# Kernel tuning notes

Hardware: AMD Instinct MI355X
Metric: run time of the kernel (lower is better)

## Reference

```python
import jax, jax.numpy as jnp
import numpy as np

N_NODES = 50000
N_EDGES = 800000
NODE_DIM = 128
EDGE_DIM = 128
HIDDEN = 128
GATE_DIM = 2


def _mlp(x, w1, b1, w2, b2):
    # Linear -> ReLU -> Linear (assumed 2-layer MLP(in, out, hidden))
    return jax.nn.relu(x @ w1.T + b1) @ w2.T + b2


def _init_linear(key, out_d, in_d, scale=0.02):
    return (jax.random.normal(key, (out_d, in_d), dtype=jnp.float32) * scale)


def setup_inputs() -> dict:
    key = jax.random.key(0)
    ks = jax.random.split(key, 32)
    inp = {}
    inp["h_node"] = jax.random.normal(ks[0], (N_NODES, NODE_DIM), dtype=jnp.float32)
    inp["h_edge"] = jax.random.normal(ks[1], (N_EDGES, EDGE_DIM), dtype=jnp.float32)
    inp["edge_index"] = jax.random.randint(ks[2], (2, N_EDGES), 0, N_NODES, dtype=jnp.int64)
    inp["relative_vec"] = jax.random.normal(ks[3], (N_EDGES, 3), dtype=jnp.float32)
    inp["distance"] = jax.random.uniform(ks[4], (N_EDGES,), dtype=jnp.float32)
    inp["node_extra"] = jax.random.normal(ks[5], (N_NODES, GATE_DIM), dtype=jnp.float32)
    # left_lin_edge: MLP(node_dim, node_dim, hidden)
    inp["left_w1"] = _init_linear(ks[6], HIDDEN, NODE_DIM)
    inp["left_b1"] = jnp.zeros((HIDDEN,), jnp.float32)
    inp["left_w2"] = _init_linear(ks[7], NODE_DIM, HIDDEN)
    inp["left_b2"] = jnp.zeros((NODE_DIM,), jnp.float32)
    # right_lin_edge: MLP(node_dim, node_dim, hidden)
    inp["right_w1"] = _init_linear(ks[8], HIDDEN, NODE_DIM)
    inp["right_b1"] = jnp.zeros((HIDDEN,), jnp.float32)
    inp["right_w2"] = _init_linear(ks[9], NODE_DIM, HIDDEN)
    inp["right_b2"] = jnp.zeros((NODE_DIM,), jnp.float32)
    # BondFFN(edge_dim, node_dim*2, inter_dim=node_dim, gate_dim, out_dim=1)
    inp["bond_lin_w"] = _init_linear(ks[10], NODE_DIM, EDGE_DIM)           # bond_linear (no bias)
    inp["nodeb_lin_w"] = _init_linear(ks[11], NODE_DIM, 2 * NODE_DIM)      # node_linear (no bias)
    inp["inter_w1"] = _init_linear(ks[12], NODE_DIM, NODE_DIM)             # inter MLP(node_dim,1,node_dim)
    inp["inter_b1"] = jnp.zeros((NODE_DIM,), jnp.float32)
    inp["inter_w2"] = _init_linear(ks[13], 1, NODE_DIM)
    inp["inter_b2"] = jnp.zeros((1,), jnp.float32)
    gate_in = EDGE_DIM + 2 * NODE_DIM + GATE_DIM                            # 386
    inp["gate_w1"] = _init_linear(ks[14], 32, gate_in)                     # gate MLP(gate_in,1,32)
    inp["gate_b1"] = jnp.zeros((32,), jnp.float32)
    inp["gate_w2"] = _init_linear(ks[15], 1, 32)
    inp["gate_b2"] = jnp.zeros((1,), jnp.float32)
    # pos_scale_net: MLP(node_dim+1+2, 1, hidden) -> sigmoid
    inp["scale_w1"] = _init_linear(ks[16], HIDDEN, NODE_DIM + 1 + GATE_DIM)
    inp["scale_b1"] = jnp.zeros((HIDDEN,), jnp.float32)
    inp["scale_w2"] = _init_linear(ks[17], 1, HIDDEN)
    inp["scale_b2"] = jnp.zeros((1,), jnp.float32)
    return inp


def reference(h_node, h_edge, edge_index, relative_vec, distance, node_extra,
              left_w1, left_b1, left_w2, left_b2,
              right_w1, right_b1, right_w2, right_b2,
              bond_lin_w, nodeb_lin_w,
              inter_w1, inter_b1, inter_w2, inter_b2,
              gate_w1, gate_b1, gate_w2, gate_b2,
              scale_w1, scale_b1, scale_w2, scale_b2):
    el, er = edge_index[0], edge_index[1]
    # gather + per-edge node MLPs
    left_feat = _mlp(h_node[el], left_w1, left_b1, left_w2, left_b2)    # [E, node_dim]
    right_feat = _mlp(h_node[er], right_w1, right_b1, right_w2, right_b2)
    both_extra = node_extra[el]                                         # [E, gate_dim]
    node_cat = jnp.concatenate([left_feat, right_feat], axis=-1)        # [E, 2*node_dim]
    # BondFFN
    inter_feat = h_edge @ bond_lin_w.T + node_cat @ nodeb_lin_w.T       # [E, node_dim]
    inter_feat = _mlp(inter_feat, inter_w1, inter_b1, inter_w2, inter_b2)  # [E, 1]
    gate = _mlp(jnp.concatenate([h_edge, node_cat, both_extra], axis=-1),
                gate_w1, gate_b1, gate_w2, gate_b2)                     # [E, 1]
    weight_edge = inter_feat * jax.nn.sigmoid(gate)                     # [E, 1]
    d = distance[:, None]
    force_edge = weight_edge * relative_vec / (d + 1e-6) / (d + 5.0) * 5  # [E, 3]
    # scatter_sum over left node index
    delta_pos = jax.ops.segment_sum(force_edge, el, num_segments=h_node.shape[0])  # [N, 3]
    nrm = jnp.linalg.norm(delta_pos, axis=-1, keepdims=True)
    scale = jax.nn.sigmoid(_mlp(jnp.concatenate([h_node, node_extra, nrm], axis=-1),
                                scale_w1, scale_b1, scale_w2, scale_b2))  # [N, 1]
    return delta_pos * scale
```

## Files before the change

### kernel.cpp

```cpp
#include <hip/hip_runtime.h>
#include <math.h>

#define N_NODES 50000
#define N_EDGES 800000

using bf16x8 = __attribute__((ext_vector_type(8))) short;
using f32x4  = __attribute__((ext_vector_type(4))) float;
typedef unsigned short u16;
typedef unsigned int   u32;

__device__ __forceinline__ u16 f2bf(float f) {
    union { float f; u32 u; } v; v.f = f;
    u32 u = v.u + 0x7fffu + ((v.u >> 16) & 1u);
    return (u16)(u >> 16);
}
__device__ __forceinline__ float bf2f(u32 h) {
    union { u32 u; float f; } v; v.u = h << 16;
    return v.f;
}

#define SA_LD 136
#define SW_LD 40

template<bool RELU>
__global__ __launch_bounds__(256, 4)
void mfma_gemm(const u16* __restrict__ A, int lda,
               const u16* __restrict__ W, int ldw,
               const float* __restrict__ bias,
               u16* __restrict__ C, int ldc,
               int M, int N, int K)
{
    __shared__ u16 sA[64 * SW_LD];
    __shared__ u16 sW[64 * SW_LD];
    const int tid = threadIdx.x;
    const int w = tid >> 6, lane = tid & 63, lx = lane & 15, quad = lane >> 4;
    const int m0 = blockIdx.x * 64, n0 = blockIdx.y * 64;

    f32x4 acc[4];
#pragma unroll
    for (int nt = 0; nt < 4; ++nt) {
        float b = bias ? bias[n0 + nt * 16 + lx] : 0.f;
        f32x4 t; t[0] = b; t[1] = b; t[2] = b; t[3] = b; acc[nt] = t;
    }

    const int sr = tid >> 2;
    const int sseg = (tid & 3) * 8;
    const int ksteps = K >> 5;
    for (int ks = 0; ks < ksteps; ++ks) {
        const int k0 = ks * 32;
        __syncthreads();
        int am = m0 + sr; if (am >= M) am = M - 1;
        uint4 va = *(const uint4*)&A[(size_t)am * lda + k0 + sseg];
        *(uint4*)&sA[sr * SW_LD + sseg] = va;
        uint4 vw = *(const uint4*)&W[(size_t)(n0 + sr) * ldw + k0 + sseg];
        *(uint4*)&sW[sr * SW_LD + sseg] = vw;
        __syncthreads();
        bf16x8 af = *(const bf16x8*)&sA[(w * 16 + lx) * SW_LD + quad * 8];
#pragma unroll
        for (int nt = 0; nt < 4; ++nt) {
            bf16x8 bf = *(const bf16x8*)&sW[(nt * 16 + lx) * SW_LD + quad * 8];
            acc[nt] = __builtin_amdgcn_mfma_f32_16x16x32_bf16(af, bf, acc[nt], 0, 0, 0);
        }
    }
#pragma unroll
    for (int r = 0; r < 4; ++r) {
        int m = m0 + w * 16 + quad * 4 + r;
        if (m >= M) continue;
#pragma unroll
        for (int nt = 0; nt < 4; ++nt) {
            float v = acc[nt][r];
            if (RELU) v = fmaxf(v, 0.f);
            C[(size_t)m * ldc + n0 + nt * 16 + lx] = f2bf(v);
        }
    }
}

__global__ void conv_hnode(const float* __restrict__ src, u16* __restrict__ dst)
{
    int idx = blockIdx.x * 256 + threadIdx.x;
    if (idx >= N_NODES * 32) return;
    float4 v = ((const float4*)src)[idx];
    uint2 o;
    o.x = (u32)f2bf(v.x) | ((u32)f2bf(v.y) << 16);
    o.y = (u32)f2bf(v.z) | ((u32)f2bf(v.w) << 16);
    *(uint2*)&dst[(size_t)idx * 4] = o;
}

__global__ void prep_small(const float* lw1, const float* rw1,
                           const float* lb1, const float* rb1,
                           const float* bond_w, const float* iw1, const float* gw1,
                           const float* sw1,
                           u16* W1cat, float* b1cat, u16* bond_bf, u16* iw1_bf,
                           u16* gate_bf, u16* sw1c)
{
    int idx = blockIdx.x * 256 + threadIdx.x;
    if (idx < 32768) {
        int i = idx >> 7, k = idx & 127;
        float v = (i < 128) ? lw1[i * 128 + k] : rw1[(i - 128) * 128 + k];
        W1cat[idx] = f2bf(v);
    } else if (idx < 33024) {
        int i = idx - 32768;
        b1cat[i] = (i < 128) ? lb1[i] : rb1[i - 128];
    } else if (idx < 49408) {
        int t = idx - 33024;
        int e = t & 7, lx = (t >> 3) & 15, quad = (t >> 7) & 3;
        int ks = (t >> 9) & 3, g = t >> 11;
        int n = g * 16 + lx, k = ks * 32 + quad * 8 + e;
        bond_bf[t] = f2bf(bond_w[n * 128 + k]);
    } else if (idx < 65792) {
        int t = idx - 49408;
        int e = t & 7, lx = (t >> 3) & 15, quad = (t >> 7) & 3;
        int ks = (t >> 9) & 3, g = t >> 11;
        int n = g * 16 + lx, k = ks * 32 + quad * 8 + e;
        iw1_bf[t] = f2bf(iw1[n * 128 + k]);
    } else if (idx < 69888) {
        int t = idx - 65792;
        int e = t & 7, lx = (t >> 3) & 15, quad = (t >> 7) & 3;
        int ks = (t >> 9) & 3, g = t >> 11;
        int n = g * 16 + lx, k = ks * 32 + quad * 8 + e;
        gate_bf[t] = f2bf(gw1[(size_t)n * 386 + k]);
    } else if (idx < 90368) {
        int t = idx - 69888;
        int o = t / 160, k = t % 160;
        sw1c[t] = (k < 131) ? f2bf(sw1[(size_t)o * 131 + k]) : (u16)0;
    }
}

__global__ void compose_wp(const float* __restrict__ nodeb_w, const float* __restrict__ gw1,
                           const float* __restrict__ lw2, const float* __restrict__ rw2,
                           const float* __restrict__ lb2, const float* __restrict__ rb2,
                           const float* __restrict__ gb1,
                           u16* __restrict__ WP, float* __restrict__ bP)
{
    int idx = blockIdx.x * 256 + threadIdx.x;
    if (idx >= 320 * 256) return;
    int i = idx >> 8;
    int j = idx & 255;
    bool leftRow = (i < 160);
    bool leftK = (j < 128);
    if (leftRow != leftK) { WP[idx] = 0; return; }

    const float* src;
    const float* w2 = leftRow ? lw2 : rw2;
    const float* b2 = leftRow ? lb2 : rb2;
    float biasExtra = 0.f;
    if (i < 128) {
        int c = ((i & 7) << 4) + (i >> 3);
        src = nodeb_w + (size_t)c * 256;
    } else if (i < 160) {
        int r = i - 128, g = ((r & 1) << 4) + (r >> 1);
        src = gw1 + (size_t)g * 386 + 128;
        biasExtra = gb1[g];
    } else if (i < 288) {
        int r = i - 160, c = ((r & 7) << 4) + (r >> 3);
        src = nodeb_w + (size_t)c * 256 + 128;
    } else {
        int r = i - 288, g = ((r & 1) << 4) + (r >> 1);
        src = gw1 + (size_t)g * 386 + 256;
    }
    int jj = j & 127;
    float s = 0.f;
#pragma unroll 4
    for (int k = 0; k < 128; ++k)
        s += src[k] * w2[(size_t)k * 128 + jj];
    WP[idx] = f2bf(s);
    if (jj == 0) {
        float b = biasExtra;
        for (int k = 0; k < 128; ++k) b += src[k] * b2[k];
        bP[i] = b;
    }
}

__global__ void fix_glx(u16* __restrict__ P, const float* __restrict__ ne,
                        const float* __restrict__ gw1)
{
    int idx = blockIdx.x * 256 + threadIdx.x;
    if (idx >= N_NODES * 32) return;
    int n = idx >> 5, g = idx & 31;
    int pos = ((g & 15) << 1) + (g >> 4);
    u16* p = &P[(size_t)n * 320 + 128 + pos];
    float v = bf2f(*p) + ne[n * 2] * gw1[(size_t)g * 386 + 384]
                       + ne[n * 2 + 1] * gw1[(size_t)g * 386 + 385];
    *p = f2bf(v);
}

__global__ __launch_bounds__(512, 4)
void edge_kernel(const float* __restrict__ he,
                 const int*   __restrict__ eidx,
                 const float* __restrict__ rel_vec,
                 const float* __restrict__ dist,
                 const u16*   __restrict__ P,
                 const u16*   __restrict__ bondw,
                 const u16*   __restrict__ iw1w,
                 const u16*   __restrict__ gatew,
                 const float* __restrict__ ib1,
                 const float* __restrict__ iw2,
                 const float* __restrict__ ib2,
                 const float* __restrict__ gw2,
                 const float* __restrict__ gb2,
                 float* __restrict__ dp)
{
    __shared__ u16 sA[128 * SA_LD];
    __shared__ u16 sW[16384 + 4096];
    __shared__ int sEL[128], sER[128];
    __shared__ float sG[128], sIS[128];

    const int tid = threadIdx.x;
    const int w = tid >> 6, lane = tid & 63, lx = lane & 15, quad = lane >> 4;
    const int eb = blockIdx.x * 128;

    if (tid < 128) { sEL[tid] = eidx[eb + tid]; sER[tid] = eidx[N_EDGES + eb + tid]; }

#pragma unroll
    for (int j = 0; j < 4; ++j) {
        int t = j * 512 + tid;
        *(uint4*)&sW[t * 8] = *(const uint4*)&bondw[t * 8];
    }
    *(uint4*)&sW[16384 + tid * 8] = *(const uint4*)&gatew[tid * 8];

#pragma unroll
    for (int j = 0; j < 8; ++j) {
        int fid = j * 512 + tid;
        int e = fid >> 5, kq = (fid & 31) << 2;
        float4 v = *(const float4*)&he[(size_t)(eb + e) * 128 + kq];
        uint2 o;
        o.x = (u32)f2bf(v.x) | ((u32)f2bf(v.y) << 16);
        o.y = (u32)f2bf(v.z) | ((u32)f2bf(v.w) << 16);
        *(uint2*)&sA[e * SA_LD + kq] = o;
    }
    __syncthreads();

    uint4 lv[4], rv[4]; u32 gl[4], gr[4];
#pragma unroll
    for (int r = 0; r < 4; ++r) {
        int erow = w * 16 + quad * 4 + r;
        size_t lbase = (size_t)sEL[erow] * 320;
        size_t rbase = (size_t)sER[erow] * 320 + 160;
        lv[r] = *(const uint4*)&P[lbase + lx * 8];
        rv[r] = *(const uint4*)&P[rbase + lx * 8];
        gl[r] = *(const u32*)&P[lbase + 128 + lx * 2];
        gr[r] = *(const u32*)&P[rbase + 128 + lx * 2];
    }

    f32x4 acc[8], accg[2];
#pragma unroll
    for (int i = 0; i < 8; ++i) { f32x4 z; z[0]=0;z[1]=0;z[2]=0;z[3]=0; acc[i] = z; }
    { f32x4 z; z[0]=0;z[1]=0;z[2]=0;z[3]=0; accg[0] = z; accg[1] = z; }

#pragma unroll
    for (int ks = 0; ks < 4; ++ks) {
        bf16x8 af = *(const bf16x8*)&sA[(w * 16 + lx) * SA_LD + ks * 32 + quad * 8];
#pragma unroll
        for (int nt = 0; nt < 8; ++nt) {
            bf16x8 bf = *(const bf16x8*)&sW[((nt * 4 + ks) << 9) + lane * 8];
            acc[nt] = __builtin_amdgcn_mfma_f32_16x16x32_bf16(af, bf, acc[nt], 0, 0, 0);
        }
#pragma unroll
        for (int nt = 0; nt < 2; ++nt) {
            bf16x8 bf = *(const bf16x8*)&sW[16384 + ((nt * 4 + ks) << 9) + lane * 8];
            accg[nt] = __builtin_amdgcn_mfma_f32_16x16x32_bf16(af, bf, accg[nt], 0, 0, 0);
        }
    }

    {
        float gw2a = gw2[lx], gw2b = gw2[16 + lx];
        float gb2v = gb2[0];
#pragma unroll
        for (int r = 0; r < 4; ++r) {
            float g0 = bf2f(gl[r] & 0xffff) + bf2f(gr[r] & 0xffff);
            float g1 = bf2f(gl[r] >> 16) + bf2f(gr[r] >> 16);
            float v = fmaxf(accg[0][r] + g0, 0.f) * gw2a
                    + fmaxf(accg[1][r] + g1, 0.f) * gw2b;
            v += __shfl_xor(v, 1); v += __shfl_xor(v, 2);
            v += __shfl_xor(v, 4); v += __shfl_xor(v, 8);
            if (lx == 0) sG[w * 16 + quad * 4 + r] = 1.f / (1.f + __expf(-(v + gb2v)));
        }
    }

#pragma unroll
    for (int r = 0; r < 4; ++r) {
        int erow = w * 16 + quad * 4 + r;
        const u32* lw_ = (const u32*)&lv[r];
        const u32* rw_ = (const u32*)&rv[r];
#pragma unroll
        for (int nt = 0; nt < 8; ++nt) {
            u32 lh = (nt & 1) ? (lw_[nt >> 1] >> 16) : (lw_[nt >> 1] & 0xffff);
            u32 rh = (nt & 1) ? (rw_[nt >> 1] >> 16) : (rw_[nt >> 1] & 0xffff);
            float tv = acc[nt][r] + bf2f(lh) + bf2f(rh);
            sA[erow * SA_LD + nt * 16 + lx] = f2bf(tv);
        }
    }
#pragma unroll
    for (int nt = 0; nt < 8; ++nt) {
        float b = ib1[nt * 16 + lx];
        f32x4 t; t[0] = b; t[1] = b; t[2] = b; t[3] = b; acc[nt] = t;
    }

    __syncthreads();
#pragma unroll
    for (int j = 0; j < 4; ++j) {
        int t = j * 512 + tid;
        *(uint4*)&sW[t * 8] = *(const uint4*)&iw1w[t * 8];
    }
    __syncthreads();

#pragma unroll
    for (int ks = 0; ks < 4; ++ks) {
        bf16x8 af = *(const bf16x8*)&sA[(w * 16 + lx) * SA_LD + ks * 32 + quad * 8];
#pragma unroll
        for (int nt = 0; nt < 8; ++nt) {
            bf16x8 bf = *(const bf16x8*)&sW[((nt * 4 + ks) << 9) + lane * 8];
            acc[nt] = __builtin_amdgcn_mfma_f32_16x16x32_bf16(af, bf, acc[nt], 0, 0, 0);
        }
    }

    {
        float ib2v = ib2[0];
        float iw2v[8];
#pragma unroll
        for (int nt = 0; nt < 8; ++nt) iw2v[nt] = iw2[nt * 16 + lx];
#pragma unroll
        for (int r = 0; r < 4; ++r) {
            float v = 0.f;
#pragma unroll
            for (int nt = 0; nt < 8; ++nt)
                v += fmaxf(acc[nt][r], 0.f) * iw2v[nt];
            v += __shfl_xor(v, 1); v += __shfl_xor(v, 2);
            v += __shfl_xor(v, 4); v += __shfl_xor(v, 8);
            if (lx == 0) sIS[w * 16 + quad * 4 + r] = v + ib2v;
        }
    }
    __syncthreads();

    {
        int e = tid >> 2, c = tid & 3;
        if (c < 3) {
            float wgt = sIS[e] * sG[e];
            float d = dist[eb + e];
            float coef = 5.f * wgt / ((d + 1e-6f) * (d + 5.f));
            atomicAdd(&dp[sEL[e] * 3 + c], coef * rel_vec[(size_t)(eb + e) * 3 + c]);
        }
    }
}

__global__ void build_xc(u16* __restrict__ Xc, const float* __restrict__ h_node,
                         const float* __restrict__ ne, const float* __restrict__ dp)
{
    int idx = blockIdx.x * 256 + threadIdx.x;
    if (idx >= N_NODES * 160) return;
    int n = idx / 160, c = idx % 160;
    float v;
    if (c < 128) v = h_node[(size_t)n * 128 + c];
    else if (c == 128) v = ne[n * 2];
    else if (c == 129) v = ne[n * 2 + 1];
    else if (c == 130) {
        float x = dp[n * 3], y = dp[n * 3 + 1], z = dp[n * 3 + 2];
        v = sqrtf(x * x + y * y + z * z);
    } else v = 0.f;
    Xc[idx] = f2bf(v);
}

__global__ __launch_bounds__(256)
void finalize(const u16* __restrict__ U, const float* __restrict__ sw2,
              const float* __restrict__ sb2, const float* __restrict__ dp,
              float* __restrict__ out)
{
    int node = blockIdx.x * 4 + (threadIdx.x >> 6);
    int lane = threadIdx.x & 63;
    const u16* u = &U[(size_t)node * 128];
    float p = bf2f(u[lane]) * sw2[lane] + bf2f(u[lane + 64]) * sw2[lane + 64];
    p += __shfl_xor(p, 1);  p += __shfl_xor(p, 2);
    p += __shfl_xor(p, 4);  p += __shfl_xor(p, 8);
    p += __shfl_xor(p, 16); p += __shfl_xor(p, 32);
    if (lane == 0) {
        float s = 1.f / (1.f + __expf(-(p + sb2[0])));
        out[node * 3 + 0] = dp[node * 3 + 0] * s;
        out[node * 3 + 1] = dp[node * 3 + 1] * s;
        out[node * 3 + 2] = dp[node * 3 + 2] * s;
    }
}

extern "C" void kernel_launch(void* const* d_in, const int* in_sizes, int n_in,
                              void* d_out, int out_size, void* d_ws, size_t ws_size,
                              hipStream_t stream)
{
    const float* h_node  = (const float*)d_in[0];
    const float* h_edge  = (const float*)d_in[1];
    const int*   eidx    = (const int*)  d_in[2];
    const float* rel_vec = (const float*)d_in[3];
    const float* dist    = (const float*)d_in[4];
    const float* ne      = (const float*)d_in[5];
    const float* lw1 = (const float*)d_in[6];  const float* lb1 = (const float*)d_in[7];
    const float* lw2 = (const float*)d_in[8];  const float* lb2 = (const float*)d_in[9];
    const float* rw1 = (const float*)d_in[10]; const float* rb1 = (const float*)d_in[11];
    const float* rw2 = (const float*)d_in[12]; const float* rb2 = (const float*)d_in[13];
    const float* bond_w  = (const float*)d_in[14];
    const float* nodeb_w = (const float*)d_in[15];
    const float* iw1 = (const float*)d_in[16]; const float* ib1 = (const float*)d_in[17];
    const float* iw2 = (const float*)d_in[18]; const float* ib2 = (const float*)d_in[19];
    const float* gw1 = (const float*)d_in[20]; const float* gb1 = (const float*)d_in[21];
    const float* gw2 = (const float*)d_in[22]; const float* gb2 = (const float*)d_in[23];
    const float* sw1 = (const float*)d_in[24]; const float* sb1 = (const float*)d_in[25];
    const float* sw2 = (const float*)d_in[26]; const float* sb2 = (const float*)d_in[27];
    float* out = (float*)d_out;

    char* base = (char*)d_ws;
    auto carve = [&](size_t bytes) { char* p = base; base += (bytes + 255) & ~(size_t)255; return p; };
    u16*  hnode_bf = (u16*) carve((size_t)N_NODES * 128 * 2);
    u16*  H1       = (u16*) carve((size_t)N_NODES * 256 * 2);
    u16*  P        = (u16*) carve((size_t)N_NODES * 320 * 2);
    u16*  Xc       = (u16*) carve((size_t)N_NODES * 160 * 2);
    u16*  U        = (u16*) carve((size_t)N_NODES * 128 * 2);
    u16*  W1cat    = (u16*) carve(256 * 128 * 2);
    u16*  WP       = (u16*) carve(320 * 256 * 2);
    u16*  bond_bf  = (u16*) carve(128 * 128 * 2);
    u16*  iw1_bf   = (u16*) carve(128 * 128 * 2);
    u16*  gate_bf  = (u16*) carve(32 * 128 * 2);
    u16*  sw1c     = (u16*) carve(128 * 160 * 2);
    float* b1cat   = (float*)carve(256 * 4);
    float* bP      = (float*)carve(320 * 4);
    float* dp      = (float*)carve((size_t)N_NODES * 3 * 4);

    hipMemsetAsync(dp, 0, (size_t)N_NODES * 3 * 4, stream);

    dim3 blk(256);
    conv_hnode<<<(N_NODES * 32 + 255) / 256, blk, 0, stream>>>(h_node, hnode_bf);
    prep_small<<<(90368 + 255) / 256, blk, 0, stream>>>(lw1, rw1, lb1, rb1, bond_w, iw1, gw1, sw1,
                                                        W1cat, b1cat, bond_bf, iw1_bf, gate_bf, sw1c);
    compose_wp<<<320, blk, 0, stream>>>(nodeb_w, gw1, lw2, rw2, lb2, rb2, gb1, WP, bP);

    const int MB = (N_NODES + 63) / 64;
    mfma_gemm<true ><<<dim3(MB, 4), blk, 0, stream>>>(hnode_bf, 128, W1cat, 128, b1cat, H1, 256, N_NODES, 256, 128);
    mfma_gemm<false><<<dim3(MB, 5), blk, 0, stream>>>(H1, 256, WP, 256, bP, P, 320, N_NODES, 320, 256);
    fix_glx<<<(N_NODES * 32 + 255) / 256, blk, 0, stream>>>(P, ne, gw1);

    edge_kernel<<<N_EDGES / 128, dim3(512), 0, stream>>>(h_edge, eidx, rel_vec, dist, P,
                                                         bond_bf, iw1_bf, gate_bf,
                                                         ib1, iw2, ib2, gw2, gb2, dp);

    build_xc<<<(N_NODES * 160 + 255) / 256, blk, 0, stream>>>(Xc, h_node, ne, dp);
    mfma_gemm<true ><<<dim3(MB, 2), blk, 0, stream>>>(Xc, 160, sw1c, 160, sb1, U, 128, N_NODES, 128, 160);
    finalize<<<N_NODES / 4, blk, 0, stream>>>(U, sw2, sb2, dp, out);
}
```

Before: 818.1 us.

## Fuse bf16 conversion, gate extra term and scale MLP; shard scatter atomics

Folds the h_node fp32-to-bf16 conversion into the first GEMM's load path. It moves the node_extra gate contribution from a separate fix_glx pass into the edge kernel, and pre-sums the left and right projections before the epilogue. The scatter-add now goes into 8 replicated slots selected by block index, which spreads out atomic contention. A single fused scale_kernel sums the slots, builds the concatenated input, runs the MFMA and the output MLP, replacing build_xc, a GEMM and finalize. In exchange it adds extra memset and read traffic for 8 dp copies, one extra bf16 rounding of the left plus right sum, and more shared memory in the new kernel.

Measured after the change: 803.4 us. Within noise of the previous version (-1.8%).

```diff
diff --git a/kernel.cpp b/kernel.cpp
--- a/kernel.cpp
+++ b/kernel.cpp
@@ -3,6 +3,7 @@
 
 #define N_NODES 50000
 #define N_EDGES 800000
+#define NSLOT 8
 
 using bf16x8 = __attribute__((ext_vector_type(8))) short;
 using f32x4  = __attribute__((ext_vector_type(4))) float;
@@ -21,10 +22,11 @@
 
 #define SA_LD 136
 #define SW_LD 40
-
-template<bool RELU>
+#define SC_LD 168
+
+template<bool RELU, bool AF32>
 __global__ __launch_bounds__(256, 4)
-void mfma_gemm(const u16* __restrict__ A, int lda,
+void mfma_gemm(const void* __restrict__ Av, int lda,
                const u16* __restrict__ W, int ldw,
                const float* __restrict__ bias,
                u16* __restrict__ C, int ldc,
@@ -35,6 +37,8 @@
     const int tid = threadIdx.x;
     const int w = tid >> 6, lane = tid & 63, lx = lane & 15, quad = lane >> 4;
     const int m0 = blockIdx.x * 64, n0 = blockIdx.y * 64;
+    const u16*   A16 = (const u16*)Av;
+    const float* A32 = (const float*)Av;
 
     f32x4 acc[4];
 #pragma unroll
@@ -50,8 +54,19 @@
         const int k0 = ks * 32;
         __syncthreads();
         int am = m0 + sr; if (am >= M) am = M - 1;
-        uint4 va = *(const uint4*)&A[(size_t)am * lda + k0 + sseg];
-        *(uint4*)&sA[sr * SW_LD + sseg] = va;
+        if (AF32) {
+            float4 u0 = *(const float4*)&A32[(size_t)am * lda + k0 + sseg];
+            float4 u1 = *(const float4*)&A32[(size_t)am * lda + k0 + sseg + 4];
+            uint4 o;
+            o.x = (u32)f2bf(u0.x) | ((u32)f2bf(u0.y) << 16);
+            o.y = (u32)f2bf(u0.z) | ((u32)f2bf(u0.w) << 16);
+            o.z = (u32)f2bf(u1.x) | ((u32)f2bf(u1.y) << 16);
+            o.w = (u32)f2bf(u1.z) | ((u32)f2bf(u1.w) << 16);
+            *(uint4*)&sA[sr * SW_LD + sseg] = o;
+        } else {
+            uint4 va = *(const uint4*)&A16[(size_t)am * lda + k0 + sseg];
+            *(uint4*)&sA[sr * SW_LD + sseg] = va;
+        }
         uint4 vw = *(const uint4*)&W[(size_t)(n0 + sr) * ldw + k0 + sseg];
         *(uint4*)&sW[sr * SW_LD + sseg] = vw;
         __syncthreads();
@@ -73,17 +88,6 @@
             C[(size_t)m * ldc + n0 + nt * 16 + lx] = f2bf(v);
         }
     }
-}
-
-__global__ void conv_hnode(const float* __restrict__ src, u16* __restrict__ dst)
-{
-    int idx = blockIdx.x * 256 + threadIdx.x;
-    if (idx >= N_NODES * 32) return;
-    float4 v = ((const float4*)src)[idx];
-    uint2 o;
-    o.x = (u32)f2bf(v.x) | ((u32)f2bf(v.y) << 16);
-    o.y = (u32)f2bf(v.z) | ((u32)f2bf(v.w) << 16);
-    *(uint2*)&dst[(size_t)idx * 4] = o;
 }
 
 __global__ void prep_small(const float* lw1, const float* rw1,
@@ -91,7 +95,7 @@
                            const float* bond_w, const float* iw1, const float* gw1,
                            const float* sw1,
                            u16* W1cat, float* b1cat, u16* bond_bf, u16* iw1_bf,
-                           u16* gate_bf, u16* sw1c)
+                           u16* gate_bf, u16* sw1c, float* ce)
 {
     int idx = blockIdx.x * 256 + threadIdx.x;
     if (idx < 32768) {
@@ -123,6 +127,10 @@
         int t = idx - 69888;
         int o = t / 160, k = t % 160;
         sw1c[t] = (k < 131) ? f2bf(sw1[(size_t)o * 131 + k]) : (u16)0;
+    } else if (idx < 90432) {
+        int t = idx - 90368;
+        int g = t >> 1, c = t & 1;
+        ce[t] = gw1[(size_t)g * 386 + 384 + c];
     }
 }
 
@@ -171,19 +179,6 @@
     }
 }
 
-__global__ void fix_glx(u16* __restrict__ P, const float* __restrict__ ne,
-                        const float* __restrict__ gw1)
-{
-    int idx = blockIdx.x * 256 + threadIdx.x;
-    if (idx >= N_NODES * 32) return;
-    int n = idx >> 5, g = idx & 31;
-    int pos = ((g & 15) << 1) + (g >> 4);
-    u16* p = &P[(size_t)n * 320 + 128 + pos];
-    float v = bf2f(*p) + ne[n * 2] * gw1[(size_t)g * 386 + 384]
-                       + ne[n * 2 + 1] * gw1[(size_t)g * 386 + 385];
-    *p = f2bf(v);
-}
-
 __global__ __launch_bounds__(512, 4)
 void edge_kernel(const float* __restrict__ he,
                  const int*   __restrict__ eidx,
@@ -198,6 +193,8 @@
                  const float* __restrict__ ib2,
                  const float* __restrict__ gw2,
                  const float* __restrict__ gb2,
+                 const float* __restrict__ ne,
+                 const float* __restrict__ ce,
                  float* __restrict__ dp)
 {
     __shared__ u16 sA[128 * SA_LD];
@@ -230,16 +227,26 @@
     }
     __syncthreads();
 
-    uint4 lv[4], rv[4]; u32 gl[4], gr[4];
+    uint4 lsum[4]; u32 gl[4], gr[4];
 #pragma unroll
     for (int r = 0; r < 4; ++r) {
         int erow = w * 16 + quad * 4 + r;
         size_t lbase = (size_t)sEL[erow] * 320;
         size_t rbase = (size_t)sER[erow] * 320 + 160;
-        lv[r] = *(const uint4*)&P[lbase + lx * 8];
-        rv[r] = *(const uint4*)&P[rbase + lx * 8];
+        uint4 lv = *(const uint4*)&P[lbase + lx * 8];
+        uint4 rv = *(const uint4*)&P[rbase + lx * 8];
         gl[r] = *(const u32*)&P[lbase + 128 + lx * 2];
         gr[r] = *(const u32*)&P[rbase + 128 + lx * 2];
+        const u32* lw_ = (const u32*)&lv;
+        const u32* rw_ = (const u32*)&rv;
+        uint4 o; u32* op = (u32*)&o;
+#pragma unroll
+        for (int q = 0; q < 4; ++q) {
+            float lo = bf2f(lw_[q] & 0xffff) + bf2f(rw_[q] & 0xffff);
+            float hi = bf2f(lw_[q] >> 16) + bf2f(rw_[q] >> 16);
+            op[q] = (u32)f2bf(lo) | ((u32)f2bf(hi) << 16);
+        }
+        lsum[r] = o;
     }
 
     f32x4 acc[8], accg[2];
@@ -263,30 +270,34 @@
     }
 
     {
+        const float2* ce2 = (const float2*)ce;
+        float2 cA = ce2[lx], cB = ce2[16 + lx];
         float gw2a = gw2[lx], gw2b = gw2[16 + lx];
         float gb2v = gb2[0];
 #pragma unroll
         for (int r = 0; r < 4; ++r) {
-            float g0 = bf2f(gl[r] & 0xffff) + bf2f(gr[r] & 0xffff);
-            float g1 = bf2f(gl[r] >> 16) + bf2f(gr[r] >> 16);
+            int erow = w * 16 + quad * 4 + r;
+            float2 nv = *(const float2*)&ne[(size_t)sEL[erow] * 2];
+            float g0 = bf2f(gl[r] & 0xffff) + bf2f(gr[r] & 0xffff)
+                     + nv.x * cA.x + nv.y * cA.y;
+            float g1 = bf2f(gl[r] >> 16) + bf2f(gr[r] >> 16)
+                     + nv.x * cB.x + nv.y * cB.y;
             float v = fmaxf(accg[0][r] + g0, 0.f) * gw2a
                     + fmaxf(accg[1][r] + g1, 0.f) * gw2b;
             v += __shfl_xor(v, 1); v += __shfl_xor(v, 2);
             v += __shfl_xor(v, 4); v += __shfl_xor(v, 8);
-            if (lx == 0) sG[w * 16 + quad * 4 + r] = 1.f / (1.f + __expf(-(v + gb2v)));
+            if (lx == 0) sG[erow] = 1.f / (1.f + __expf(-(v + gb2v)));
         }
     }
 
 #pragma unroll
     for (int r = 0; r < 4; ++r) {
         int erow = w * 16 + quad * 4 + r;
-        const u32* lw_ = (const u32*)&lv[r];
-        const u32* rw_ = (const u32*)&rv[r];
+        const u32* sw_ = (const u32*)&lsum[r];
 #pragma unroll
         for (int nt = 0; nt < 8; ++nt) {
-            u32 lh = (nt & 1) ? (lw_[nt >> 1] >> 16) : (lw_[nt >> 1] & 0xffff);
-            u32 rh = (nt & 1) ? (rw_[nt >> 1] >> 16) : (rw_[nt >> 1] & 0xffff);
-            float tv = acc[nt][r] + bf2f(lh) + bf2f(rh);
+            u32 h = (nt & 1) ? (sw_[nt >> 1] >> 16) : (sw_[nt >> 1] & 0xffff);
+            float tv = acc[nt][r] + bf2f(h);
             sA[erow * SA_LD + nt * 16 + lx] = f2bf(tv);
         }
     }
@@ -333,50 +344,108 @@
     __syncthreads();
 
     {
+        float* dps = dp + (size_t)(blockIdx.x & (NSLOT - 1)) * (3 * N_NODES);
         int e = tid >> 2, c = tid & 3;
         if (c < 3) {
             float wgt = sIS[e] * sG[e];
             float d = dist[eb + e];
             float coef = 5.f * wgt / ((d + 1e-6f) * (d + 5.f));
-            atomicAdd(&dp[sEL[e] * 3 + c], coef * rel_vec[(size_t)(eb + e) * 3 + c]);
-        }
-    }
-}
-
-__global__ void build_xc(u16* __restrict__ Xc, const float* __restrict__ h_node,
-                         const float* __restrict__ ne, const float* __restrict__ dp)
+            atomicAdd(&dps[sEL[e] * 3 + c], coef * rel_vec[(size_t)(eb + e) * 3 + c]);
+        }
+    }
+}
+
+__global__ __launch_bounds__(256, 4)
+void scale_kernel(const float* __restrict__ h_node,
+                  const float* __restrict__ ne,
+                  const float* __restrict__ dp,
+                  const u16*   __restrict__ sw1c,
+                  const float* __restrict__ sb1,
+                  const float* __restrict__ sw2,
+                  const float* __restrict__ sb2,
+                  float* __restrict__ out)
 {
-    int idx = blockIdx.x * 256 + threadIdx.x;
-    if (idx >= N_NODES * 160) return;
-    int n = idx / 160, c = idx % 160;
-    float v;
-    if (c < 128) v = h_node[(size_t)n * 128 + c];
-    else if (c == 128) v = ne[n * 2];
-    else if (c == 129) v = ne[n * 2 + 1];
-    else if (c == 130) {
-        float x = dp[n * 3], y = dp[n * 3 + 1], z = dp[n * 3 + 2];
-        v = sqrtf(x * x + y * y + z * z);
-    } else v = 0.f;
-    Xc[idx] = f2bf(v);
-}
-
-__global__ __launch_bounds__(256)
-void finalize(const u16* __restrict__ U, const float* __restrict__ sw2,
-              const float* __restrict__ sb2, const float* __restrict__ dp,
-              float* __restrict__ out)
-{
-    int node = blockIdx.x * 4 + (threadIdx.x >> 6);
-    int lane = threadIdx.x & 63;
-    const u16* u = &U[(size_t)node * 128];
-    float p = bf2f(u[lane]) * sw2[lane] + bf2f(u[lane + 64]) * sw2[lane + 64];
-    p += __shfl_xor(p, 1);  p += __shfl_xor(p, 2);
-    p += __shfl_xor(p, 4);  p += __shfl_xor(p, 8);
-    p += __shfl_xor(p, 16); p += __shfl_xor(p, 32);
-    if (lane == 0) {
-        float s = 1.f / (1.f + __expf(-(p + sb2[0])));
-        out[node * 3 + 0] = dp[node * 3 + 0] * s;
-        out[node * 3 + 1] = dp[node * 3 + 1] * s;
-        out[node * 3 + 2] = dp[node * 3 + 2] * s;
+    __shared__ u16 sA[64 * SC_LD];
+    __shared__ u16 sW[128 * SC_LD];
+    __shared__ float sDP[64][3];
+    const int tid = threadIdx.x;
+    const int w = tid >> 6, lane = tid & 63, lx = lane & 15, quad = lane >> 4;
+    const int m0 = blockIdx.x * 64;
+
+#pragma unroll
+    for (int j = 0; j < 4; ++j) {
+        int id = j * 256 + tid;
+        int r = id >> 4, c8 = (id & 15) << 3;
+        int am = m0 + r; if (am >= N_NODES) am = N_NODES - 1;
+        float4 u0 = *(const float4*)&h_node[(size_t)am * 128 + c8];
+        float4 u1 = *(const float4*)&h_node[(size_t)am * 128 + c8 + 4];
+        uint4 o;
+        o.x = (u32)f2bf(u0.x) | ((u32)f2bf(u0.y) << 16);
+        o.y = (u32)f2bf(u0.z) | ((u32)f2bf(u0.w) << 16);
+        o.z = (u32)f2bf(u1.x) | ((u32)f2bf(u1.y) << 16);
+        o.w = (u32)f2bf(u1.z) | ((u32)f2bf(u1.w) << 16);
+        *(uint4*)&sA[r * SC_LD + c8] = o;
+    }
+#pragma unroll
+    for (int j = 0; j < 10; ++j) {
+        int id = j * 256 + tid;
+        int r = id / 20, c8 = (id % 20) * 8;
+        *(uint4*)&sW[r * SC_LD + c8] = *(const uint4*)&sw1c[r * 160 + c8];
+    }
+    if (tid < 64) {
+        int am = m0 + tid; if (am >= N_NODES) am = N_NODES - 1;
+        float sx = 0.f, sy = 0.f, sz = 0.f;
+#pragma unroll
+        for (int s = 0; s < NSLOT; ++s) {
+            const float* d = dp + (size_t)s * (3 * N_NODES) + (size_t)am * 3;
+            sx += d[0]; sy += d[1]; sz += d[2];
+        }
+        sDP[tid][0] = sx; sDP[tid][1] = sy; sDP[tid][2] = sz;
+        float2 nv = *(const float2*)&ne[(size_t)am * 2];
+        u16* row = &sA[tid * SC_LD];
+        row[128] = f2bf(nv.x); row[129] = f2bf(nv.y);
+        row[130] = f2bf(sqrtf(sx * sx + sy * sy + sz * sz));
+#pragma unroll
+        for (int c = 131; c < 160; ++c) row[c] = 0;
+    }
+
+    f32x4 acc[8];
+#pragma unroll
+    for (int nt = 0; nt < 8; ++nt) {
+        float b = sb1[nt * 16 + lx];
+        f32x4 t; t[0] = b; t[1] = b; t[2] = b; t[3] = b; acc[nt] = t;
+    }
+    __syncthreads();
+
+#pragma unroll
+    for (int ks = 0; ks < 5; ++ks) {
+        bf16x8 af = *(const bf16x8*)&sA[(w * 16 + lx) * SC_LD + ks * 32 + quad * 8];
+#pragma unroll
+        for (int nt = 0; nt < 8; ++nt) {
+            bf16x8 bf = *(const bf16x8*)&sW[(nt * 16 + lx) * SC_LD + ks * 32 + quad * 8];
+            acc[nt] = __builtin_amdgcn_mfma_f32_16x16x32_bf16(af, bf, acc[nt], 0, 0, 0);
+        }
+    }
+
+    float sw2v[8];
+#pragma unroll
+    for (int nt = 0; nt < 8; ++nt) sw2v[nt] = sw2[nt * 16 + lx];
+    float sb2v = sb2[0];
+#pragma unroll
+    for (int r = 0; r < 4; ++r) {
+        int m = m0 + w * 16 + quad * 4 + r;
+        float v = 0.f;
+#pragma unroll
+        for (int nt = 0; nt < 8; ++nt) v += fmaxf(acc[nt][r], 0.f) * sw2v[nt];
+        v += __shfl_xor(v, 1); v += __shfl_xor(v, 2);
+        v += __shfl_xor(v, 4); v += __shfl_xor(v, 8);
+        if (lx == 0 && m < N_NODES) {
+            float s = 1.f / (1.f + __expf(-(v + sb2v)));
+            int lr = w * 16 + quad * 4 + r;
+            out[m * 3 + 0] = sDP[lr][0] * s;
+            out[m * 3 + 1] = sDP[lr][1] * s;
+            out[m * 3 + 2] = sDP[lr][2] * s;
+        }
     }
 }
 
@@ -406,39 +475,33 @@
 
     char* base = (char*)d_ws;
     auto carve = [&](size_t bytes) { char* p = base; base += (bytes + 255) & ~(size_t)255; return p; };
-    u16*  hnode_bf = (u16*) carve((size_t)N_NODES * 128 * 2);
-    u16*  H1       = (u16*) carve((size_t)N_NODES * 256 * 2);
-    u16*  P        = (u16*) carve((size_t)N_NODES * 320 * 2);
-    u16*  Xc       = (u16*) carve((size_t)N_NODES * 160 * 2);
-    u16*  U        = (u16*) carve((size_t)N_NODES * 128 * 2);
-    u16*  W1cat    = (u16*) carve(256 * 128 * 2);
-    u16*  WP       = (u16*) carve(320 * 256 * 2);
-    u16*  bond_bf  = (u16*) carve(128 * 128 * 2);
-    u16*  iw1_bf   = (u16*) carve(128 * 128 * 2);
-    u16*  gate_bf  = (u16*) carve(32 * 128 * 2);
-    u16*  sw1c     = (u16*) carve(128 * 160 * 2);
-    float* b1cat   = (float*)carve(256 * 4);
-    float* bP      = (float*)carve(320 * 4);
-    float* dp      = (float*)carve((size_t)N_NODES * 3 * 4);
-
-    hipMemsetAsync(dp, 0, (size_t)N_NODES * 3 * 4, stream);
+    u16*  H1      = (u16*) carve((size_t)N_NODES * 256 * 2);
+    u16*  P       = (u16*) carve((size_t)N_NODES * 320 * 2);
+    u16*  W1cat   = (u16*) carve(256 * 128 * 2);
+    u16*  WP      = (u16*) carve(320 * 256 * 2);
+    u16*  bond_bf = (u16*) carve(128 * 128 * 2);
+    u16*  iw1_bf  = (u16*) carve(128 * 128 * 2);
+    u16*  gate_bf = (u16*) carve(32 * 128 * 2);
+    u16*  sw1c    = (u16*) carve(128 * 160 * 2);
+    float* b1cat  = (float*)carve(256 * 4);
+    float* bP     = (float*)carve(320 * 4);
+    float* ce     = (float*)carve(64 * 4);
+    float* dp     = (float*)carve((size_t)NSLOT * N_NODES * 3 * 4);
+
+    hipMemsetAsync(dp, 0, (size_t)NSLOT * N_NODES * 3 * 4, stream);
 
     dim3 blk(256);
-    conv_hnode<<<(N_NODES * 32 + 255) / 256, blk, 0, stream>>>(h_node, hnode_bf);
-    prep_small<<<(90368 + 255) / 256, blk, 0, stream>>>(lw1, rw1, lb1, rb1, bond_w, iw1, gw1, sw1,
-                                                        W1cat, b1cat, bond_bf, iw1_bf, gate_bf, sw1c);
+    prep_small<<<(90432 + 255) / 256, blk, 0, stream>>>(lw1, rw1, lb1, rb1, bond_w, iw1, gw1, sw1,
+                                                        W1cat, b1cat, bond_bf, iw1_bf, gate_bf, sw1c, ce);
     compose_wp<<<320, blk, 0, stream>>>(nodeb_w, gw1, lw2, rw2, lb2, rb2, gb1, WP, bP);
 
     const int MB = (N_NODES + 63) / 64;
-    mfma_gemm<true ><<<dim3(MB, 4), blk, 0, stream>>>(hnode_bf, 128, W1cat, 128, b1cat, H1, 256, N_NODES, 256, 128);
-    mfma_gemm<false><<<dim3(MB, 5), blk, 0, stream>>>(H1, 256, WP, 256, bP, P, 320, N_NODES, 320, 256);
-    fix_glx<<<(N_NODES * 32 + 255) / 256, blk, 0, stream>>>(P, ne, gw1);
+    mfma_gemm<true, true ><<<dim3(MB, 4), blk, 0, stream>>>(h_node, 128, W1cat, 128, b1cat, H1, 256, N_NODES, 256, 128);
+    mfma_gemm<false, false><<<dim3(MB, 5), blk, 0, stream>>>(H1, 256, WP, 256, bP, P, 320, N_NODES, 320, 256);
 
     edge_kernel<<<N_EDGES / 128, dim3(512), 0, stream>>>(h_edge, eidx, rel_vec, dist, P,
                                                          bond_bf, iw1_bf, gate_bf,
-                                                         ib1, iw2, ib2, gw2, gb2, dp);
-
-    build_xc<<<(N_NODES * 160 + 255) / 256, blk, 0, stream>>>(Xc, h_node, ne, dp);
-    mfma_gemm<true ><<<dim3(MB, 2), blk, 0, stream>>>(Xc, 160, sw1c, 160, sb1, U, 128, N_NODES, 128, 160);
-    finalize<<<N_NODES / 4, blk, 0, stream>>>(U, sw2, sb2, dp, out);
-}
+                                                         ib1, iw2, ib2, gw2, gb2, ne, ce, dp);
+
+    scale_kernel<<<MB, blk, 0, stream>>>(h_node, ne, dp, sw1c, sb1, sw2, sb2, out);
+}
```
